# Kernel optimization log

Hardware: AMD Instinct MI355X
Metric: run time of the kernel (lower is better)

Reference implementation:

```python
import jax, jax.numpy as jnp
import numpy as np

E = 200000          # number of edges
MUL = 32            # multiplicity per irrep in irreps_in1/irreps_out
NT = 2              # num_tensors_in1
U = MUL * NT        # 64: combined multiplicity after fuse_in
SCALAR_DIM = 64     # irreps_edge_scalars num_irreps
HID = 64            # radial MLP hidden width
WNUM = 2 * U        # 128: LinearScaleWithWeights weight_numel (64 for 0e + 64 for 1o)
PW = 0.125          # uvw path weight sqrt(dim_out/ (u*v)) combined with 3j: all paths -> 1/8
INV_S3 = 1.0 / np.sqrt(3.0)

# e3nn normalize2mom constant for silu: 1/sqrt(E[silu(z)^2]), z ~ N(0,1)
_z = np.linspace(-12.0, 12.0, 200001)
_phi = np.exp(-0.5 * _z ** 2) / np.sqrt(2.0 * np.pi)
_s = _z / (1.0 + np.exp(-_z))
SILU_CST = float(1.0 / np.sqrt(np.trapz(_s ** 2 * _phi, _z)))


def setup_inputs() -> dict:
    key = jax.random.key(0)
    ks = jax.random.split(key, 15)
    f32 = jnp.float32
    return {
        "x1a": jax.random.normal(ks[0], (E, 128), f32),   # 32x0e + 32x1o
        "x1b": jax.random.normal(ks[1], (E, 128), f32),
        "x2": jax.random.normal(ks[2], (E, 4), f32),      # 1x0e + 1x1o
        "scalars": jax.random.normal(ks[3], (E, SCALAR_DIM), f32),
        # main tensor-product weights, one (u=64, w=32) block per instruction (v=1 squeezed)
        "w0": jax.random.normal(ks[4], (U, MUL), f32),    # 0e x 0e -> 0e (slot 0)
        "w1": jax.random.normal(ks[5], (U, MUL), f32),    # 1o x 1o -> 0e (slot 1)
        "w2": jax.random.normal(ks[6], (U, MUL), f32),    # 0e x 1o -> 1o (slot 2)
        "w3": jax.random.normal(ks[7], (U, MUL), f32),    # 1o x 0e -> 1o (slot 3)
        # LinearScaleWithWeights.linear_out: 64x0e+64x1o -> 32x0e+32x1o
        "Wl0": jax.random.normal(ks[8], (U, MUL), f32),
        "Wl1": jax.random.normal(ks[9], (U, MUL), f32),
        # radial MLP (e3nn FullyConnectedNet [64,64,64,128], silu)
        "Wm1": jax.random.normal(ks[10], (SCALAR_DIM, HID), f32),
        "Wm2": jax.random.normal(ks[11], (HID, HID), f32),
        "Wm3": jax.random.normal(ks[12], (HID, WNUM), f32),
        # final o3.Linear: 32x0e+32x1o -> 32x0e+32x1o
        "Wf0": jax.random.normal(ks[13], (MUL, MUL), f32),
        "Wf1": jax.random.normal(ks[14], (MUL, MUL), f32),
    }


def reference(x1a, x1b, x2, scalars, w0, w1, w2, w3, Wl0, Wl1, Wm1, Wm2, Wm3, Wf0, Wf1):
    n = x1a.shape[0]
    # fuse_in: stack heads then regroup per irrep -> combined 64x0e + 64x1o layout
    s0 = jnp.concatenate([x1a[:, :MUL], x1b[:, :MUL]], axis=1)                    # [E, 64]
    s1 = jnp.concatenate([x1a[:, MUL:].reshape(n, MUL, 3),
                          x1b[:, MUL:].reshape(n, MUL, 3)], axis=1)               # [E, 64, 3]
    y0 = x2[:, 0:1]    # 1x0e
    y1 = x2[:, 1:4]    # 1x1o

    # weight generator: e3nn FullyConnectedNet with normalized silu
    h = SILU_CST * jax.nn.silu((scalars @ Wm1) / jnp.sqrt(jnp.float32(SCALAR_DIM)))
    h = SILU_CST * jax.nn.silu((h @ Wm2) / jnp.sqrt(jnp.float32(HID)))
    weights = (h @ Wm3) / jnp.sqrt(jnp.float32(HID))                              # [E, 128]

    # main TensorProduct -> irreps_mid = 32x0e + 32x0e + 32x1o + 32x1o
    mid0 = PW * jnp.einsum('eu,uw->ew', s0 * y0, w0)                              # [E, 32]
    mid1 = (PW * INV_S3) * jnp.einsum('eu,uw->ew',
                                      jnp.einsum('euk,ek->eu', s1, y1), w1)       # [E, 32]
    mid2 = PW * jnp.einsum('eu,uw,ek->ewk', s0, w2, y1)                           # [E, 32, 3]
    mid3 = PW * jnp.einsum('euk,uw->ewk', s1 * y0[:, :, None], w3)                # [E, 32, 3]
    m0 = jnp.concatenate([mid0, mid1], axis=1)                                    # [E, 64] 0e
    m1 = jnp.concatenate([mid2, mid3], axis=1)                                    # [E, 64, 3] 1o

    # LinearScaleWithWeights: per-edge elementwise scale (uvu tp vs ones), then o3.Linear
    m0 = m0 * weights[:, :U]
    m1 = m1 * weights[:, U:, None]
    o0 = jnp.einsum('eu,uw->ew', m0, Wl0) / jnp.sqrt(jnp.float32(U))              # [E, 32]
    o1 = jnp.einsum('euk,uw->ewk', m1, Wl1) / jnp.sqrt(jnp.float32(U))            # [E, 32, 3]

    # final o3.Linear on irreps_out
    o0 = jnp.einsum('eu,uw->ew', o0, Wf0) / jnp.sqrt(jnp.float32(MUL))
    o1 = jnp.einsum('euk,uw->ewk', o1, Wf1) / jnp.sqrt(jnp.float32(MUL))
    return jnp.concatenate([o0, o1.reshape(n, MUL * 3)], axis=1)                  # [E, 128]
```

## Files before the change

kernel.cpp:

```cpp
#include <hip/hip_runtime.h>
#include <math.h>


#define TPB 256
#define ET  64
#define SAS 68

#define FMA4(acc, s, b)                                         \
  acc.x = fmaf((s), (b).x, acc.x); acc.y = fmaf((s), (b).y, acc.y); \
  acc.z = fmaf((s), (b).z, acc.z); acc.w = fmaf((s), (b).w, acc.w)

__global__ void zero_cst_kernel(double* cst) {
  if (threadIdx.x == 0) cst[0] = 0.0;
}

__global__ void cst_accum_kernel(double* cst) {
  __shared__ double red[256];
  double sum = 0.0;
  for (long i = (long)blockIdx.x * 256 + threadIdx.x; i <= 200000; i += 64L * 256) {
    double z = -12.0 + (double)i * (24.0 / 200000.0);
    double s = z / (1.0 + exp(-z));
    double phi = exp(-0.5 * z * z) * 0.3989422804014327;
    double f = s * s * phi;
    if (i == 0 || i == 200000) f *= 0.5;
    sum += f;
  }
  red[threadIdx.x] = sum;
  __syncthreads();
  for (int off = 128; off > 0; off >>= 1) {
    if (threadIdx.x < (unsigned)off) red[threadIdx.x] += red[threadIdx.x + off];
    __syncthreads();
  }
  if (threadIdx.x == 0) atomicAdd(cst, red[0]);
}

__global__ void prep_C_kernel(const float* __restrict__ Wl0, const float* __restrict__ Wf0,
                              const float* __restrict__ Wl1, const float* __restrict__ Wf1,
                              float* __restrict__ C0, float* __restrict__ C1) {
  const float* Wl = blockIdx.x ? Wl1 : Wl0;
  const float* Wf = blockIdx.x ? Wf1 : Wf0;
  float* C = blockIdx.x ? C1 : C0;
  for (int i = threadIdx.x; i < 64 * 32; i += 256) {
    int u = i >> 5, w = i & 31;
    float acc = 0.f;
#pragma unroll
    for (int v = 0; v < 32; ++v) acc = fmaf(Wl[u * 32 + v], Wf[v * 32 + w], acc);
    C[i] = acc * 0.022097086912079612f;
  }
}

__device__ __forceinline__ void stageB(const float* __restrict__ g, int ncols, int col0,
                                       float* __restrict__ sB, int t) {
#pragma unroll
  for (int r = 0; r < 2; ++r) {
    int i = (r * TPB + t) * 4;
    int c = i >> 5, j = i & 31;
    *(float4*)(sB + i) = *(const float4*)(g + c * ncols + col0 + j);
  }
}

__device__ __forceinline__ void gemm2(const float* __restrict__ sA,
                                      const float* __restrict__ sB,
                                      int e0l, int e1l, int cg,
                                      float4& out0, float4& out1) {
  float4 acc0 = make_float4(0.f, 0.f, 0.f, 0.f);
  float4 acc1 = make_float4(0.f, 0.f, 0.f, 0.f);
  const float* a0p = sA + e0l * SAS;
  const float* a1p = sA + e1l * SAS;
  const float* bp  = sB + 4 * cg;
#pragma unroll 4
  for (int c4 = 0; c4 < 16; ++c4) {
    float4 a0 = *(const float4*)(a0p + 4 * c4);
    float4 a1 = *(const float4*)(a1p + 4 * c4);
    const float* bb = bp + c4 * 128;
    float4 b0 = *(const float4*)(bb);
    float4 b1 = *(const float4*)(bb + 32);
    float4 b2 = *(const float4*)(bb + 64);
    float4 b3 = *(const float4*)(bb + 96);
    FMA4(acc0, a0.x, b0); FMA4(acc1, a1.x, b0);
    FMA4(acc0, a0.y, b1); FMA4(acc1, a1.y, b1);
    FMA4(acc0, a0.z, b2); FMA4(acc1, a1.z, b2);
    FMA4(acc0, a0.w, b3); FMA4(acc1, a1.w, b3);
  }
  out0 = acc0;
  out1 = acc1;
}

__device__ __forceinline__ float silu1(float x, float cst) {
  x *= 0.125f;
  return cst * x / (1.f + __expf(-x));
}

__device__ __forceinline__ float4 siluq(float4 v, float cst) {
  return make_float4(silu1(v.x, cst), silu1(v.y, cst), silu1(v.z, cst), silu1(v.w, cst));
}

__device__ __forceinline__ float4 muls(float4 a, float s) {
  return make_float4(a.x * s, a.y * s, a.z * s, a.w * s);
}

__device__ __forceinline__ float4 cmul(float4 a, float4 b, float s) {
  return make_float4(s * a.x * b.x, s * a.y * b.y, s * a.z * b.z, s * a.w * b.w);
}

__global__ __launch_bounds__(TPB, 4) void fused_tp(
    const float* __restrict__ x1a, const float* __restrict__ x1b,
    const float* __restrict__ x2, const float* __restrict__ scalars,
    const float* __restrict__ w0, const float* __restrict__ w1,
    const float* __restrict__ w2, const float* __restrict__ w3,
    const float* __restrict__ Wm1, const float* __restrict__ Wm2,
    const float* __restrict__ Wm3, const float* __restrict__ C0,
    const float* __restrict__ C1, const double* __restrict__ cstp,
    float* __restrict__ out) {
  __shared__ float sA[ET * SAS];
  __shared__ float sB0[64 * 32];
  __shared__ float sB1[64 * 32];
  __shared__ float sY[ET * 4];

  const int t  = threadIdx.x;
  const int cg = t & 7;
  const int eh = t >> 3;
  const long e0 = (long)blockIdx.x * ET;
  const float cst = (float)(1.0 / sqrt(cstp[0] * (24.0 / 200000.0)));

  const float pw   = 0.125f;
  const float pws3 = 0.125f * 0.57735026918962576f;

  if (t < ET) *(float4*)(sY + 4 * t) = *(const float4*)(x2 + (e0 + t) * 4);
#pragma unroll
  for (int r = 0; r < 4; ++r) {
    int i = r * TPB + t; int e = i >> 4; int j4 = (i & 15) << 2;
    *(float4*)(sA + e * SAS + j4) = *(const float4*)(scalars + (e0 + e) * 64 + j4);
  }
  stageB(Wm1, 64, 0, sB0, t);
  stageB(Wm1, 64, 32, sB1, t);
  __syncthreads();

  float4 h0a, h0b, h1a, h1b;
  {
    float4 r0, r1;
    gemm2(sA, sB0, eh, eh + 32, cg, r0, r1);
    h0a = siluq(r0, cst); h1a = siluq(r1, cst);
    gemm2(sA, sB1, eh, eh + 32, cg, r0, r1);
    h0b = siluq(r0, cst); h1b = siluq(r1, cst);
  }
  __syncthreads();

  *(float4*)(sA + eh * SAS + 4 * cg)        = h0a;
  *(float4*)(sA + eh * SAS + 32 + 4 * cg)   = h0b;
  *(float4*)(sA + (eh + 32) * SAS + 4 * cg)      = h1a;
  *(float4*)(sA + (eh + 32) * SAS + 32 + 4 * cg) = h1b;
  stageB(Wm2, 64, 0, sB0, t);
  stageB(Wm2, 64, 32, sB1, t);
  __syncthreads();

  {
    float4 r0, r1;
    gemm2(sA, sB0, eh, eh + 32, cg, r0, r1);
    h0a = siluq(r0, cst); h1a = siluq(r1, cst);
    gemm2(sA, sB1, eh, eh + 32, cg, r0, r1);
    h0b = siluq(r0, cst); h1b = siluq(r1, cst);
  }
  __syncthreads();

  *(float4*)(sA + eh * SAS + 4 * cg)        = h0a;
  *(float4*)(sA + eh * SAS + 32 + 4 * cg)   = h0b;
  *(float4*)(sA + (eh + 32) * SAS + 4 * cg)      = h1a;
  *(float4*)(sA + (eh + 32) * SAS + 32 + 4 * cg) = h1b;
  stageB(Wm3, 128, 0, sB0, t);
  stageB(Wm3, 128, 32, sB1, t);
  __syncthreads();

  float4 wq[2][4];
  {
    float4 r0, r1;
    gemm2(sA, sB0, eh, eh + 32, cg, r0, r1);
    wq[0][0] = muls(r0, 0.125f); wq[1][0] = muls(r1, 0.125f);
    gemm2(sA, sB1, eh, eh + 32, cg, r0, r1);
    wq[0][1] = muls(r0, 0.125f); wq[1][1] = muls(r1, 0.125f);
  }
  __syncthreads();
  stageB(Wm3, 128, 64, sB0, t);
  stageB(Wm3, 128, 96, sB1, t);
  __syncthreads();
  {
    float4 r0, r1;
    gemm2(sA, sB0, eh, eh + 32, cg, r0, r1);
    wq[0][2] = muls(r0, 0.125f); wq[1][2] = muls(r1, 0.125f);
    gemm2(sA, sB1, eh, eh + 32, cg, r0, r1);
    wq[0][3] = muls(r0, 0.125f); wq[1][3] = muls(r1, 0.125f);
  }
  __syncthreads();

#pragma unroll
  for (int r = 0; r < 4; ++r) {
    int i = r * TPB + t; int e = i >> 4; int j4 = (i & 15) << 2;
    const float* src = (j4 < 32) ? (x1a + (e0 + e) * 128 + j4)
                                 : (x1b + (e0 + e) * 128 + j4 - 32);
    *(float4*)(sA + e * SAS + j4) = *(const float4*)src;
  }
  stageB(w0, 32, 0, sB0, t);
  stageB(w2, 32, 0, sB1, t);
  __syncthreads();
  float4 m0q[2], p2q[2];
  gemm2(sA, sB0, eh, eh + 32, cg, m0q[0], m0q[1]);
  gemm2(sA, sB1, eh, eh + 32, cg, p2q[0], p2q[1]);
  __syncthreads();

#pragma unroll 2
  for (int r = 0; r < 16; ++r) {
    int i = r * TPB + t; int e = i >> 6; int u = i & 63;
    const float* xr = ((u < 32) ? x1a : x1b) + (e0 + e) * 128 + 32 + 3 * (u & 31);
    const float* yr = sY + e * 4;
    sA[e * SAS + u] = xr[0] * yr[1] + xr[1] * yr[2] + xr[2] * yr[3];
  }
  stageB(w1, 32, 0, sB0, t);
  stageB(w3, 32, 0, sB1, t);
  __syncthreads();
  float4 m1q[2];
  gemm2(sA, sB0, eh, eh + 32, cg, m1q[0], m1q[1]);
  __syncthreads();

#pragma unroll
  for (int ei = 0; ei < 2; ++ei) {
    int e = eh + 32 * ei;
    float y0v = sY[e * 4];
    *(float4*)(sA + e * SAS + 4 * cg)      = cmul(m0q[ei], wq[ei][0], pw * y0v);
    *(float4*)(sA + e * SAS + 32 + 4 * cg) = cmul(m1q[ei], wq[ei][1], pws3);
  }
  stageB(C0, 32, 0, sB0, t);
  __syncthreads();
  float4 o0q[2];
  gemm2(sA, sB0, eh, eh + 32, cg, o0q[0], o0q[1]);
  __syncthreads();

  stageB(C1, 32, 0, sB0, t);
  float o1v[2][12];
#pragma unroll
  for (int k = 0; k < 3; ++k) {
#pragma unroll 2
    for (int r = 0; r < 16; ++r) {
      int i = r * TPB + t; int e = i >> 6; int u = i & 63;
      const float* xr = ((u < 32) ? x1a : x1b) + (e0 + e) * 128 + 32 + 3 * (u & 31);
      sA[e * SAS + u] = xr[k];
    }
    __syncthreads();
    float4 t3[2];
    gemm2(sA, sB1, eh, eh + 32, cg, t3[0], t3[1]);
    __syncthreads();
#pragma unroll
    for (int ei = 0; ei < 2; ++ei) {
      int e = eh + 32 * ei;
      float y0v = sY[e * 4];
      float y1k = sY[e * 4 + 1 + k];
      *(float4*)(sA + e * SAS + 4 * cg)      = cmul(p2q[ei], wq[ei][2], pw * y1k);
      *(float4*)(sA + e * SAS + 32 + 4 * cg) = cmul(t3[ei], wq[ei][3], pw * y0v);
    }
    __syncthreads();
    float4 r0, r1;
    gemm2(sA, sB0, eh, eh + 32, cg, r0, r1);
    o1v[0][0 + k] = r0.x; o1v[0][3 + k] = r0.y; o1v[0][6 + k] = r0.z; o1v[0][9 + k] = r0.w;
    o1v[1][0 + k] = r1.x; o1v[1][3 + k] = r1.y; o1v[1][6 + k] = r1.z; o1v[1][9 + k] = r1.w;
    __syncthreads();
  }

#pragma unroll
  for (int ei = 0; ei < 2; ++ei) {
    long eg = e0 + eh + 32 * ei;
    float* ob = out + eg * 128;
    *(float4*)(ob + 4 * cg) = o0q[ei];
    float* o1b = ob + 32 + 12 * cg;
    *(float4*)(o1b)     = make_float4(o1v[ei][0], o1v[ei][1], o1v[ei][2],  o1v[ei][3]);
    *(float4*)(o1b + 4) = make_float4(o1v[ei][4], o1v[ei][5], o1v[ei][6],  o1v[ei][7]);
    *(float4*)(o1b + 8) = make_float4(o1v[ei][8], o1v[ei][9], o1v[ei][10], o1v[ei][11]);
  }
}

extern "C" void kernel_launch(void* const* d_in, const int* in_sizes, int n_in,
                              void* d_out, int out_size, void* d_ws, size_t ws_size,
                              hipStream_t stream) {
  const float* x1a     = (const float*)d_in[0];
  const float* x1b     = (const float*)d_in[1];
  const float* x2      = (const float*)d_in[2];
  const float* scalars = (const float*)d_in[3];
  const float* w0      = (const float*)d_in[4];
  const float* w1      = (const float*)d_in[5];
  const float* w2      = (const float*)d_in[6];
  const float* w3      = (const float*)d_in[7];
  const float* Wl0     = (const float*)d_in[8];
  const float* Wl1     = (const float*)d_in[9];
  const float* Wm1     = (const float*)d_in[10];
  const float* Wm2     = (const float*)d_in[11];
  const float* Wm3     = (const float*)d_in[12];
  const float* Wf0     = (const float*)d_in[13];
  const float* Wf1     = (const float*)d_in[14];
  float* out = (float*)d_out;

  double* cst = (double*)d_ws;
  float* C0 = (float*)d_ws + 128;
  float* C1 = C0 + 64 * 32;

  const int E = in_sizes[0] / 128;
  const int nblocks = E / ET;

  zero_cst_kernel<<<1, 64, 0, stream>>>(cst);
  cst_accum_kernel<<<64, 256, 0, stream>>>(cst);
  prep_C_kernel<<<2, 256, 0, stream>>>(Wl0, Wf0, Wl1, Wf1, C0, C1);
  fused_tp<<<nblocks, TPB, 0, stream>>>(x1a, x1b, x2, scalars, w0, w1, w2, w3,
                                        Wm1, Wm2, Wm3, C0, C1, cst, out);
}
```

Before: 481.4 us.

## Double-buffer shared tiles, hoist mid2 GEMM out of k-loop, vectorize x1 loads

Adds double-buffered A and B shared tiles so the next weight stage loads while the current GEMM runs, which cuts the number of barriers. The mid2 product (s0·w2 then ·C1) is computed once and scaled by y1k per k instead of running through the full 64-wide GEMM three times. The 1o inputs are loaded once into registers as float4 and reused for the dot product and for each k slice, replacing strided scalar global reads. An XOR-swizzled 32-wide buffer is added for the half-size GEMMs. In exchange, shared memory and register use grow, and launch bounds drop to 2 blocks per SM, which lowers occupancy.

```diff
diff --git a/kernel.cpp b/kernel.cpp
--- a/kernel.cpp
+++ b/kernel.cpp
@@ -57,6 +57,13 @@
     int c = i >> 5, j = i & 31;
     *(float4*)(sB + i) = *(const float4*)(g + c * ncols + col0 + j);
   }
+}
+
+__device__ __forceinline__ void stageB32(const float* __restrict__ g, int row0,
+                                         float* __restrict__ sB, int t) {
+  int i = t * 4;
+  int c = i >> 5, j = i & 31;
+  *(float4*)(sB + i) = *(const float4*)(g + (row0 + c) * 32 + j);
 }
 
 __device__ __forceinline__ void gemm2(const float* __restrict__ sA,
@@ -86,6 +93,39 @@
   out1 = acc1;
 }
 
+__device__ __forceinline__ void gemm32(const float* __restrict__ sAx,
+                                       const float* __restrict__ sB,
+                                       int e0l, int e1l, int cg,
+                                       float4& out0, float4& out1) {
+  float4 acc0 = make_float4(0.f, 0.f, 0.f, 0.f);
+  float4 acc1 = make_float4(0.f, 0.f, 0.f, 0.f);
+  const float* a0p = sAx + e0l * 32;
+  const float* a1p = sAx + e1l * 32;
+  const int x0 = (e0l & 7) << 2;
+  const int x1 = (e1l & 7) << 2;
+  const float* bp  = sB + 4 * cg;
+#pragma unroll
+  for (int c4 = 0; c4 < 8; ++c4) {
+    float4 a0 = *(const float4*)(a0p + ((c4 << 2) ^ x0));
+    float4 a1 = *(const float4*)(a1p + ((c4 << 2) ^ x1));
+    const float* bb = bp + c4 * 128;
+    float4 b0 = *(const float4*)(bb);
+    float4 b1 = *(const float4*)(bb + 32);
+    float4 b2 = *(const float4*)(bb + 64);
+    float4 b3 = *(const float4*)(bb + 96);
+    FMA4(acc0, a0.x, b0); FMA4(acc1, a1.x, b0);
+    FMA4(acc0, a0.y, b1); FMA4(acc1, a1.y, b1);
+    FMA4(acc0, a0.z, b2); FMA4(acc1, a1.z, b2);
+    FMA4(acc0, a0.w, b3); FMA4(acc1, a1.w, b3);
+  }
+  out0 = acc0;
+  out1 = acc1;
+}
+
+__device__ __forceinline__ void put32(float* __restrict__ sb, int e, int cg, float4 v) {
+  *(float4*)(sb + e * 32 + ((cg ^ (e & 7)) << 2)) = v;
+}
+
 __device__ __forceinline__ float silu1(float x, float cst) {
   x *= 0.125f;
   return cst * x / (1.f + __expf(-x));
@@ -103,7 +143,29 @@
   return make_float4(s * a.x * b.x, s * a.y * b.y, s * a.z * b.z, s * a.w * b.w);
 }
 
-__global__ __launch_bounds__(TPB, 4) void fused_tp(
+#define S1K(dst, kk) do {                                                     \
+  _Pragma("unroll")                                                           \
+  for (int r = 0; r < 4; ++r) {                                               \
+    int i = r * TPB + t; int e = i >> 4; int m = i & 15;                      \
+    *(float4*)((dst) + e * SAS + 4 * m) =                                     \
+      make_float4(xw[r][kk], xw[r][3 + kk], xw[r][6 + kk], xw[r][9 + kk]);    \
+  }                                                                           \
+} while (0)
+
+#define COMBINE(kk, r0, r1) do {                                              \
+  float ya = (kk == 0) ? yv0.y : (kk == 1) ? yv0.z : yv0.w;                   \
+  float yb = (kk == 0) ? yv1.y : (kk == 1) ? yv1.z : yv1.w;                   \
+  o1v[0][kk]     = ya * q2q[0].x + (r0).x;                                    \
+  o1v[0][3 + kk] = ya * q2q[0].y + (r0).y;                                    \
+  o1v[0][6 + kk] = ya * q2q[0].z + (r0).z;                                    \
+  o1v[0][9 + kk] = ya * q2q[0].w + (r0).w;                                    \
+  o1v[1][kk]     = yb * q2q[1].x + (r1).x;                                    \
+  o1v[1][3 + kk] = yb * q2q[1].y + (r1).y;                                    \
+  o1v[1][6 + kk] = yb * q2q[1].z + (r1).z;                                    \
+  o1v[1][9 + kk] = yb * q2q[1].w + (r1).w;                                    \
+} while (0)
+
+__global__ __launch_bounds__(TPB, 2) void fused_tp(
     const float* __restrict__ x1a, const float* __restrict__ x1b,
     const float* __restrict__ x2, const float* __restrict__ scalars,
     const float* __restrict__ w0, const float* __restrict__ w1,
@@ -112,10 +174,11 @@
     const float* __restrict__ Wm3, const float* __restrict__ C0,
     const float* __restrict__ C1, const double* __restrict__ cstp,
     float* __restrict__ out) {
-  __shared__ float sA[ET * SAS];
-  __shared__ float sB0[64 * 32];
-  __shared__ float sB1[64 * 32];
-  __shared__ float sY[ET * 4];
+  __shared__ __align__(16) float sA0[ET * SAS];
+  __shared__ __align__(16) float sA1[ET * SAS];
+  __shared__ __align__(16) float sBB[4][64 * 32];
+  __shared__ __align__(16) float s32[64 * 32];
+  __shared__ __align__(16) float sY[ET * 4];
 
   const int t  = threadIdx.x;
   const int cg = t & 7;
@@ -130,140 +193,157 @@
 #pragma unroll
   for (int r = 0; r < 4; ++r) {
     int i = r * TPB + t; int e = i >> 4; int j4 = (i & 15) << 2;
-    *(float4*)(sA + e * SAS + j4) = *(const float4*)(scalars + (e0 + e) * 64 + j4);
-  }
-  stageB(Wm1, 64, 0, sB0, t);
-  stageB(Wm1, 64, 32, sB1, t);
-  __syncthreads();
-
-  float4 h0a, h0b, h1a, h1b;
-  {
-    float4 r0, r1;
-    gemm2(sA, sB0, eh, eh + 32, cg, r0, r1);
-    h0a = siluq(r0, cst); h1a = siluq(r1, cst);
-    gemm2(sA, sB1, eh, eh + 32, cg, r0, r1);
-    h0b = siluq(r0, cst); h1b = siluq(r1, cst);
-  }
-  __syncthreads();
-
-  *(float4*)(sA + eh * SAS + 4 * cg)        = h0a;
-  *(float4*)(sA + eh * SAS + 32 + 4 * cg)   = h0b;
-  *(float4*)(sA + (eh + 32) * SAS + 4 * cg)      = h1a;
-  *(float4*)(sA + (eh + 32) * SAS + 32 + 4 * cg) = h1b;
-  stageB(Wm2, 64, 0, sB0, t);
-  stageB(Wm2, 64, 32, sB1, t);
-  __syncthreads();
-
-  {
-    float4 r0, r1;
-    gemm2(sA, sB0, eh, eh + 32, cg, r0, r1);
-    h0a = siluq(r0, cst); h1a = siluq(r1, cst);
-    gemm2(sA, sB1, eh, eh + 32, cg, r0, r1);
-    h0b = siluq(r0, cst); h1b = siluq(r1, cst);
-  }
-  __syncthreads();
-
-  *(float4*)(sA + eh * SAS + 4 * cg)        = h0a;
-  *(float4*)(sA + eh * SAS + 32 + 4 * cg)   = h0b;
-  *(float4*)(sA + (eh + 32) * SAS + 4 * cg)      = h1a;
-  *(float4*)(sA + (eh + 32) * SAS + 32 + 4 * cg) = h1b;
-  stageB(Wm3, 128, 0, sB0, t);
-  stageB(Wm3, 128, 32, sB1, t);
-  __syncthreads();
-
+    *(float4*)(sA0 + e * SAS + j4) = *(const float4*)(scalars + (e0 + e) * 64 + j4);
+  }
+  stageB(Wm1, 64, 0, sBB[0], t);
+  stageB(Wm1, 64, 32, sBB[1], t);
+  __syncthreads();
+
+  const float4 yv0 = *(const float4*)(sY + eh * 4);
+  const float4 yv1 = *(const float4*)(sY + (eh + 32) * 4);
+
+  stageB(Wm2, 64, 0, sBB[2], t);
+  stageB(Wm2, 64, 32, sBB[3], t);
+  {
+    float4 r0, r1;
+    gemm2(sA0, sBB[0], eh, eh + 32, cg, r0, r1);
+    *(float4*)(sA1 + eh * SAS + 4 * cg)        = siluq(r0, cst);
+    *(float4*)(sA1 + (eh + 32) * SAS + 4 * cg) = siluq(r1, cst);
+    gemm2(sA0, sBB[1], eh, eh + 32, cg, r0, r1);
+    *(float4*)(sA1 + eh * SAS + 32 + 4 * cg)        = siluq(r0, cst);
+    *(float4*)(sA1 + (eh + 32) * SAS + 32 + 4 * cg) = siluq(r1, cst);
+  }
+  __syncthreads();
+
+  stageB(Wm3, 128, 0, sBB[0], t);
+  stageB(Wm3, 128, 32, sBB[1], t);
+  {
+    float4 r0, r1;
+    gemm2(sA1, sBB[2], eh, eh + 32, cg, r0, r1);
+    *(float4*)(sA0 + eh * SAS + 4 * cg)        = siluq(r0, cst);
+    *(float4*)(sA0 + (eh + 32) * SAS + 4 * cg) = siluq(r1, cst);
+    gemm2(sA1, sBB[3], eh, eh + 32, cg, r0, r1);
+    *(float4*)(sA0 + eh * SAS + 32 + 4 * cg)        = siluq(r0, cst);
+    *(float4*)(sA0 + (eh + 32) * SAS + 32 + 4 * cg) = siluq(r1, cst);
+  }
+  __syncthreads();
+
+  stageB(Wm3, 128, 64, sBB[2], t);
+  stageB(Wm3, 128, 96, sBB[3], t);
   float4 wq[2][4];
   {
     float4 r0, r1;
-    gemm2(sA, sB0, eh, eh + 32, cg, r0, r1);
+    gemm2(sA0, sBB[0], eh, eh + 32, cg, r0, r1);
     wq[0][0] = muls(r0, 0.125f); wq[1][0] = muls(r1, 0.125f);
-    gemm2(sA, sB1, eh, eh + 32, cg, r0, r1);
+    gemm2(sA0, sBB[1], eh, eh + 32, cg, r0, r1);
     wq[0][1] = muls(r0, 0.125f); wq[1][1] = muls(r1, 0.125f);
   }
-  __syncthreads();
-  stageB(Wm3, 128, 64, sB0, t);
-  stageB(Wm3, 128, 96, sB1, t);
-  __syncthreads();
-  {
-    float4 r0, r1;
-    gemm2(sA, sB0, eh, eh + 32, cg, r0, r1);
-    wq[0][2] = muls(r0, 0.125f); wq[1][2] = muls(r1, 0.125f);
-    gemm2(sA, sB1, eh, eh + 32, cg, r0, r1);
-    wq[0][3] = muls(r0, 0.125f); wq[1][3] = muls(r1, 0.125f);
-  }
-  __syncthreads();
-
 #pragma unroll
   for (int r = 0; r < 4; ++r) {
     int i = r * TPB + t; int e = i >> 4; int j4 = (i & 15) << 2;
     const float* src = (j4 < 32) ? (x1a + (e0 + e) * 128 + j4)
                                  : (x1b + (e0 + e) * 128 + j4 - 32);
-    *(float4*)(sA + e * SAS + j4) = *(const float4*)src;
-  }
-  stageB(w0, 32, 0, sB0, t);
-  stageB(w2, 32, 0, sB1, t);
-  __syncthreads();
+    *(float4*)(sA1 + e * SAS + j4) = *(const float4*)src;
+  }
+  __syncthreads();
+
+  stageB(w0, 32, 0, sBB[0], t);
+  stageB(w2, 32, 0, sBB[1], t);
+  float xw[4][12];
+#pragma unroll
+  for (int r = 0; r < 4; ++r) {
+    int i = r * TPB + t; int e = i >> 4; int m = i & 15;
+    const float* src = ((m < 8) ? x1a : x1b) + (e0 + e) * 128 + 32 + 12 * (m & 7);
+    float4 va = *(const float4*)(src);
+    float4 vb = *(const float4*)(src + 4);
+    float4 vc = *(const float4*)(src + 8);
+    xw[r][0] = va.x; xw[r][1]  = va.y; xw[r][2]  = va.z; xw[r][3]  = va.w;
+    xw[r][4] = vb.x; xw[r][5]  = vb.y; xw[r][6]  = vb.z; xw[r][7]  = vb.w;
+    xw[r][8] = vc.x; xw[r][9]  = vc.y; xw[r][10] = vc.z; xw[r][11] = vc.w;
+  }
+  {
+    float4 r0, r1;
+    gemm2(sA0, sBB[2], eh, eh + 32, cg, r0, r1);
+    wq[0][2] = muls(r0, 0.125f); wq[1][2] = muls(r1, 0.125f);
+    gemm2(sA0, sBB[3], eh, eh + 32, cg, r0, r1);
+    wq[0][3] = muls(r0, 0.125f); wq[1][3] = muls(r1, 0.125f);
+  }
+  __syncthreads();
+
+  stageB(w1, 32, 0, sBB[2], t);
+  stageB(w3, 32, 0, sBB[3], t);
   float4 m0q[2], p2q[2];
-  gemm2(sA, sB0, eh, eh + 32, cg, m0q[0], m0q[1]);
-  gemm2(sA, sB1, eh, eh + 32, cg, p2q[0], p2q[1]);
-  __syncthreads();
-
-#pragma unroll 2
-  for (int r = 0; r < 16; ++r) {
-    int i = r * TPB + t; int e = i >> 6; int u = i & 63;
-    const float* xr = ((u < 32) ? x1a : x1b) + (e0 + e) * 128 + 32 + 3 * (u & 31);
+  gemm2(sA1, sBB[0], eh, eh + 32, cg, m0q[0], m0q[1]);
+  gemm2(sA1, sBB[1], eh, eh + 32, cg, p2q[0], p2q[1]);
+#pragma unroll
+  for (int r = 0; r < 4; ++r) {
+    int i = r * TPB + t; int e = i >> 4; int m = i & 15;
     const float* yr = sY + e * 4;
-    sA[e * SAS + u] = xr[0] * yr[1] + xr[1] * yr[2] + xr[2] * yr[3];
-  }
-  stageB(w1, 32, 0, sB0, t);
-  stageB(w3, 32, 0, sB1, t);
-  __syncthreads();
+    float4 tv;
+    tv.x = xw[r][0] * yr[1] + xw[r][1]  * yr[2] + xw[r][2]  * yr[3];
+    tv.y = xw[r][3] * yr[1] + xw[r][4]  * yr[2] + xw[r][5]  * yr[3];
+    tv.z = xw[r][6] * yr[1] + xw[r][7]  * yr[2] + xw[r][8]  * yr[3];
+    tv.w = xw[r][9] * yr[1] + xw[r][10] * yr[2] + xw[r][11] * yr[3];
+    *(float4*)(sA0 + e * SAS + 4 * m) = tv;
+  }
+  __syncthreads();
+
+  stageB(C0, 32, 0, sBB[0], t);
+  stageB32(C1, 0, sBB[1], t);
   float4 m1q[2];
-  gemm2(sA, sB0, eh, eh + 32, cg, m1q[0], m1q[1]);
-  __syncthreads();
-
-#pragma unroll
-  for (int ei = 0; ei < 2; ++ei) {
-    int e = eh + 32 * ei;
-    float y0v = sY[e * 4];
-    *(float4*)(sA + e * SAS + 4 * cg)      = cmul(m0q[ei], wq[ei][0], pw * y0v);
-    *(float4*)(sA + e * SAS + 32 + 4 * cg) = cmul(m1q[ei], wq[ei][1], pws3);
-  }
-  stageB(C0, 32, 0, sB0, t);
-  __syncthreads();
+  gemm2(sA0, sBB[2], eh, eh + 32, cg, m1q[0], m1q[1]);
+  S1K(sA1, 0);
+  put32(s32, eh,      cg, cmul(p2q[0], wq[0][2], pw));
+  put32(s32, eh + 32, cg, cmul(p2q[1], wq[1][2], pw));
+  __syncthreads();
+
+  stageB32(C1, 32, sBB[2], t);
+  float4 t3[2], q2q[2];
+  gemm2(sA1, sBB[3], eh, eh + 32, cg, t3[0], t3[1]);
+  gemm32(s32, sBB[1], eh, eh + 32, cg, q2q[0], q2q[1]);
+  *(float4*)(sA0 + eh * SAS + 4 * cg)             = cmul(m0q[0], wq[0][0], pw * yv0.x);
+  *(float4*)(sA0 + eh * SAS + 32 + 4 * cg)        = cmul(m1q[0], wq[0][1], pws3);
+  *(float4*)(sA0 + (eh + 32) * SAS + 4 * cg)      = cmul(m0q[1], wq[1][0], pw * yv1.x);
+  *(float4*)(sA0 + (eh + 32) * SAS + 32 + 4 * cg) = cmul(m1q[1], wq[1][1], pws3);
+  __syncthreads();
+
   float4 o0q[2];
-  gemm2(sA, sB0, eh, eh + 32, cg, o0q[0], o0q[1]);
-  __syncthreads();
-
-  stageB(C1, 32, 0, sB0, t);
+  gemm2(sA0, sBB[0], eh, eh + 32, cg, o0q[0], o0q[1]);
+  put32(sBB[1], eh,      cg, cmul(t3[0], wq[0][3], pw * yv0.x));
+  put32(sBB[1], eh + 32, cg, cmul(t3[1], wq[1][3], pw * yv1.x));
+  S1K(sA1, 1);
+  __syncthreads();
+
   float o1v[2][12];
-#pragma unroll
-  for (int k = 0; k < 3; ++k) {
-#pragma unroll 2
-    for (int r = 0; r < 16; ++r) {
-      int i = r * TPB + t; int e = i >> 6; int u = i & 63;
-      const float* xr = ((u < 32) ? x1a : x1b) + (e0 + e) * 128 + 32 + 3 * (u & 31);
-      sA[e * SAS + u] = xr[k];
-    }
-    __syncthreads();
-    float4 t3[2];
-    gemm2(sA, sB1, eh, eh + 32, cg, t3[0], t3[1]);
-    __syncthreads();
-#pragma unroll
-    for (int ei = 0; ei < 2; ++ei) {
-      int e = eh + 32 * ei;
-      float y0v = sY[e * 4];
-      float y1k = sY[e * 4 + 1 + k];
-      *(float4*)(sA + e * SAS + 4 * cg)      = cmul(p2q[ei], wq[ei][2], pw * y1k);
-      *(float4*)(sA + e * SAS + 32 + 4 * cg) = cmul(t3[ei], wq[ei][3], pw * y0v);
-    }
-    __syncthreads();
-    float4 r0, r1;
-    gemm2(sA, sB0, eh, eh + 32, cg, r0, r1);
-    o1v[0][0 + k] = r0.x; o1v[0][3 + k] = r0.y; o1v[0][6 + k] = r0.z; o1v[0][9 + k] = r0.w;
-    o1v[1][0 + k] = r1.x; o1v[1][3 + k] = r1.y; o1v[1][6 + k] = r1.z; o1v[1][9 + k] = r1.w;
-    __syncthreads();
-  }
-
+  {
+    float4 r0, r1;
+    gemm32(sBB[1], sBB[2], eh, eh + 32, cg, r0, r1);
+    COMBINE(0, r0, r1);
+  }
+  gemm2(sA1, sBB[3], eh, eh + 32, cg, t3[0], t3[1]);
+  S1K(sA0, 2);
+  __syncthreads();
+
+  put32(s32, eh,      cg, cmul(t3[0], wq[0][3], pw * yv0.x));
+  put32(s32, eh + 32, cg, cmul(t3[1], wq[1][3], pw * yv1.x));
+  float4 t32a, t32b;
+  gemm2(sA0, sBB[3], eh, eh + 32, cg, t32a, t32b);
+  __syncthreads();
+
+  {
+    float4 r0, r1;
+    gemm32(s32, sBB[2], eh, eh + 32, cg, r0, r1);
+    COMBINE(1, r0, r1);
+  }
+  put32(sBB[1], eh,      cg, cmul(t32a, wq[0][3], pw * yv0.x));
+  put32(sBB[1], eh + 32, cg, cmul(t32b, wq[1][3], pw * yv1.x));
+  __syncthreads();
+
+  {
+    float4 r0, r1;
+    gemm32(sBB[1], sBB[2], eh, eh + 32, cg, r0, r1);
+    COMBINE(2, r0, r1);
+  }
 #pragma unroll
   for (int ei = 0; ei < 2; ++ei) {
     long eg = e0 + eh + 32 * ei;
```

New measurement: 1.135 ms. +135.9%, slower.

## Widen edge tile to 128 per block and restructure tensor-product GEMM stages

Applied to the files above, without the earlier changes.

The fused kernel is templated on edges per thread, and the main launch now handles 128 edges per block with 4 edges per thread. A tail launch with 2 edges per thread covers the remainder. Dual-B GEMMs share A-fragment loads across two weight matrices. The 1o path is split algebraically: the y1-dependent term is computed once through a K=32 GEMM and scaled per component k, instead of one K=64 GEMM per component. The x1 vector gathers are vectorized with float4 loads, and launch bounds drop to 3 blocks per SM. This raises register pressure and reduces occupancy, and it assumes E is a multiple of 64.

```diff
diff --git a/kernel.cpp b/kernel.cpp
--- a/kernel.cpp
+++ b/kernel.cpp
@@ -3,7 +3,6 @@
 
 
 #define TPB 256
-#define ET  64
 #define SAS 68
 
 #define FMA4(acc, s, b)                                         \
@@ -59,31 +58,99 @@
   }
 }
 
-__device__ __forceinline__ void gemm2(const float* __restrict__ sA,
-                                      const float* __restrict__ sB,
-                                      int e0l, int e1l, int cg,
-                                      float4& out0, float4& out1) {
-  float4 acc0 = make_float4(0.f, 0.f, 0.f, 0.f);
-  float4 acc1 = make_float4(0.f, 0.f, 0.f, 0.f);
-  const float* a0p = sA + e0l * SAS;
-  const float* a1p = sA + e1l * SAS;
-  const float* bp  = sB + 4 * cg;
+template <int EPT>
+__device__ __forceinline__ void gemm_one(const float* __restrict__ sA,
+                                         const float* __restrict__ sB,
+                                         int eh, int cg, float4 (&out)[EPT]) {
+  float4 acc[EPT];
+#pragma unroll
+  for (int i = 0; i < EPT; ++i) acc[i] = make_float4(0.f, 0.f, 0.f, 0.f);
+  const float* bp = sB + 4 * cg;
 #pragma unroll 4
   for (int c4 = 0; c4 < 16; ++c4) {
-    float4 a0 = *(const float4*)(a0p + 4 * c4);
-    float4 a1 = *(const float4*)(a1p + 4 * c4);
     const float* bb = bp + c4 * 128;
     float4 b0 = *(const float4*)(bb);
     float4 b1 = *(const float4*)(bb + 32);
     float4 b2 = *(const float4*)(bb + 64);
     float4 b3 = *(const float4*)(bb + 96);
-    FMA4(acc0, a0.x, b0); FMA4(acc1, a1.x, b0);
-    FMA4(acc0, a0.y, b1); FMA4(acc1, a1.y, b1);
-    FMA4(acc0, a0.z, b2); FMA4(acc1, a1.z, b2);
-    FMA4(acc0, a0.w, b3); FMA4(acc1, a1.w, b3);
-  }
-  out0 = acc0;
-  out1 = acc1;
+#pragma unroll
+    for (int i = 0; i < EPT; ++i) {
+      float4 a = *(const float4*)(sA + (eh + 32 * i) * SAS + 4 * c4);
+      FMA4(acc[i], a.x, b0);
+      FMA4(acc[i], a.y, b1);
+      FMA4(acc[i], a.z, b2);
+      FMA4(acc[i], a.w, b3);
+    }
+  }
+#pragma unroll
+  for (int i = 0; i < EPT; ++i) out[i] = acc[i];
+}
+
+template <int EPT>
+__device__ __forceinline__ void gemm_dual(const float* __restrict__ sA,
+                                          const float* __restrict__ sB0,
+                                          const float* __restrict__ sB1,
+                                          int eh, int cg,
+                                          float4 (&out0)[EPT], float4 (&out1)[EPT]) {
+  float4 a0[EPT], a1[EPT];
+#pragma unroll
+  for (int i = 0; i < EPT; ++i) {
+    a0[i] = make_float4(0.f, 0.f, 0.f, 0.f);
+    a1[i] = make_float4(0.f, 0.f, 0.f, 0.f);
+  }
+  const float* bp0 = sB0 + 4 * cg;
+  const float* bp1 = sB1 + 4 * cg;
+#pragma unroll 2
+  for (int c4 = 0; c4 < 16; ++c4) {
+    const float* b0b = bp0 + c4 * 128;
+    const float* b1b = bp1 + c4 * 128;
+    float4 B00 = *(const float4*)(b0b);
+    float4 B01 = *(const float4*)(b0b + 32);
+    float4 B02 = *(const float4*)(b0b + 64);
+    float4 B03 = *(const float4*)(b0b + 96);
+    float4 B10 = *(const float4*)(b1b);
+    float4 B11 = *(const float4*)(b1b + 32);
+    float4 B12 = *(const float4*)(b1b + 64);
+    float4 B13 = *(const float4*)(b1b + 96);
+#pragma unroll
+    for (int i = 0; i < EPT; ++i) {
+      float4 a = *(const float4*)(sA + (eh + 32 * i) * SAS + 4 * c4);
+      FMA4(a0[i], a.x, B00); FMA4(a1[i], a.x, B10);
+      FMA4(a0[i], a.y, B01); FMA4(a1[i], a.y, B11);
+      FMA4(a0[i], a.z, B02); FMA4(a1[i], a.z, B12);
+      FMA4(a0[i], a.w, B03); FMA4(a1[i], a.w, B13);
+    }
+  }
+#pragma unroll
+  for (int i = 0; i < EPT; ++i) { out0[i] = a0[i]; out1[i] = a1[i]; }
+}
+
+template <int EPT>
+__device__ __forceinline__ void gemm_k32(const float* __restrict__ sA,
+                                         const float* __restrict__ sBbase,
+                                         int eh, int cg, float4 (&out)[EPT]) {
+  float4 acc[EPT];
+#pragma unroll
+  for (int i = 0; i < EPT; ++i) acc[i] = make_float4(0.f, 0.f, 0.f, 0.f);
+  const float* bp = sBbase + 4 * cg;
+#pragma unroll 4
+  for (int c4 = 0; c4 < 8; ++c4) {
+    const float* bb = bp + c4 * 128;
+    float4 b0 = *(const float4*)(bb);
+    float4 b1 = *(const float4*)(bb + 32);
+    float4 b2 = *(const float4*)(bb + 64);
+    float4 b3 = *(const float4*)(bb + 96);
+#pragma unroll
+    for (int i = 0; i < EPT; ++i) {
+      float4 a = *(const float4*)(sA + (eh + 32 * i) * SAS + 4 * c4);
+      FMA4(acc[i], a.x, b0);
+      FMA4(acc[i], a.y, b1);
+      FMA4(acc[i], a.z, b2);
+      FMA4(acc[i], a.w, b3);
+    }
+  }
+#pragma unroll
+  for (int i = 0; i < EPT; ++i) out[i] = acc[i];
 }
 
 __device__ __forceinline__ float silu1(float x, float cst) {
@@ -103,7 +170,18 @@
   return make_float4(s * a.x * b.x, s * a.y * b.y, s * a.z * b.z, s * a.w * b.w);
 }
 
-__global__ __launch_bounds__(TPB, 4) void fused_tp(
+__device__ __forceinline__ float4 emul(float4 a, float4 b) {
+  return make_float4(a.x * b.x, a.y * b.y, a.z * b.z, a.w * b.w);
+}
+
+__device__ __forceinline__ float4 pick3(float4 va, float4 vb, float4 vc, int k) {
+  if (k == 0) return make_float4(va.x, va.w, vb.z, vc.y);
+  if (k == 1) return make_float4(va.y, vb.x, vb.w, vc.z);
+  return make_float4(va.z, vb.y, vc.x, vc.w);
+}
+
+template <int EPT>
+__global__ __launch_bounds__(TPB, 3) void fused_tp(
     const float* __restrict__ x1a, const float* __restrict__ x1b,
     const float* __restrict__ x2, const float* __restrict__ scalars,
     const float* __restrict__ w0, const float* __restrict__ w1,
@@ -111,16 +189,17 @@
     const float* __restrict__ Wm1, const float* __restrict__ Wm2,
     const float* __restrict__ Wm3, const float* __restrict__ C0,
     const float* __restrict__ C1, const double* __restrict__ cstp,
-    float* __restrict__ out) {
-  __shared__ float sA[ET * SAS];
-  __shared__ float sB0[64 * 32];
-  __shared__ float sB1[64 * 32];
-  __shared__ float sY[ET * 4];
+    float* __restrict__ out, long ebase) {
+  constexpr int ET = 32 * EPT;
+  __shared__ __align__(16) float sA[ET * SAS];
+  __shared__ __align__(16) float sB0[64 * 32];
+  __shared__ __align__(16) float sB1[64 * 32];
+  __shared__ __align__(16) float sY[ET * 4];
 
   const int t  = threadIdx.x;
   const int cg = t & 7;
   const int eh = t >> 3;
-  const long e0 = (long)blockIdx.x * ET;
+  const long e0 = ebase + (long)blockIdx.x * ET;
   const float cst = (float)(1.0 / sqrt(cstp[0] * (24.0 / 200000.0)));
 
   const float pw   = 0.125f;
@@ -128,7 +207,7 @@
 
   if (t < ET) *(float4*)(sY + 4 * t) = *(const float4*)(x2 + (e0 + t) * 4);
 #pragma unroll
-  for (int r = 0; r < 4; ++r) {
+  for (int r = 0; r < ET / 16; ++r) {
     int i = r * TPB + t; int e = i >> 4; int j4 = (i & 15) << 2;
     *(float4*)(sA + e * SAS + j4) = *(const float4*)(scalars + (e0 + e) * 64 + j4);
   }
@@ -136,64 +215,51 @@
   stageB(Wm1, 64, 32, sB1, t);
   __syncthreads();
 
-  float4 h0a, h0b, h1a, h1b;
-  {
-    float4 r0, r1;
-    gemm2(sA, sB0, eh, eh + 32, cg, r0, r1);
-    h0a = siluq(r0, cst); h1a = siluq(r1, cst);
-    gemm2(sA, sB1, eh, eh + 32, cg, r0, r1);
-    h0b = siluq(r0, cst); h1b = siluq(r1, cst);
-  }
-  __syncthreads();
-
-  *(float4*)(sA + eh * SAS + 4 * cg)        = h0a;
-  *(float4*)(sA + eh * SAS + 32 + 4 * cg)   = h0b;
-  *(float4*)(sA + (eh + 32) * SAS + 4 * cg)      = h1a;
-  *(float4*)(sA + (eh + 32) * SAS + 32 + 4 * cg) = h1b;
+  float4 yv[EPT];
+#pragma unroll
+  for (int i = 0; i < EPT; ++i) yv[i] = *(const float4*)(sY + (eh + 32 * i) * 4);
+
+  float4 g0[EPT], g1[EPT];
+
+  gemm_dual<EPT>(sA, sB0, sB1, eh, cg, g0, g1);
+  __syncthreads();
+#pragma unroll
+  for (int i = 0; i < EPT; ++i) {
+    int e = eh + 32 * i;
+    *(float4*)(sA + e * SAS + 4 * cg)      = siluq(g0[i], cst);
+    *(float4*)(sA + e * SAS + 32 + 4 * cg) = siluq(g1[i], cst);
+  }
   stageB(Wm2, 64, 0, sB0, t);
   stageB(Wm2, 64, 32, sB1, t);
   __syncthreads();
 
-  {
-    float4 r0, r1;
-    gemm2(sA, sB0, eh, eh + 32, cg, r0, r1);
-    h0a = siluq(r0, cst); h1a = siluq(r1, cst);
-    gemm2(sA, sB1, eh, eh + 32, cg, r0, r1);
-    h0b = siluq(r0, cst); h1b = siluq(r1, cst);
-  }
-  __syncthreads();
-
-  *(float4*)(sA + eh * SAS + 4 * cg)        = h0a;
-  *(float4*)(sA + eh * SAS + 32 + 4 * cg)   = h0b;
-  *(float4*)(sA + (eh + 32) * SAS + 4 * cg)      = h1a;
-  *(float4*)(sA + (eh + 32) * SAS + 32 + 4 * cg) = h1b;
+  gemm_dual<EPT>(sA, sB0, sB1, eh, cg, g0, g1);
+  __syncthreads();
+#pragma unroll
+  for (int i = 0; i < EPT; ++i) {
+    int e = eh + 32 * i;
+    *(float4*)(sA + e * SAS + 4 * cg)      = siluq(g0[i], cst);
+    *(float4*)(sA + e * SAS + 32 + 4 * cg) = siluq(g1[i], cst);
+  }
   stageB(Wm3, 128, 0, sB0, t);
   stageB(Wm3, 128, 32, sB1, t);
   __syncthreads();
 
-  float4 wq[2][4];
-  {
-    float4 r0, r1;
-    gemm2(sA, sB0, eh, eh + 32, cg, r0, r1);
-    wq[0][0] = muls(r0, 0.125f); wq[1][0] = muls(r1, 0.125f);
-    gemm2(sA, sB1, eh, eh + 32, cg, r0, r1);
-    wq[0][1] = muls(r0, 0.125f); wq[1][1] = muls(r1, 0.125f);
-  }
+  float4 wq0[EPT], wq1[EPT], wq2[EPT], wq3[EPT];
+  gemm_dual<EPT>(sA, sB0, sB1, eh, cg, g0, g1);
+#pragma unroll
+  for (int i = 0; i < EPT; ++i) { wq0[i] = muls(g0[i], 0.125f); wq1[i] = muls(g1[i], 0.125f); }
   __syncthreads();
   stageB(Wm3, 128, 64, sB0, t);
   stageB(Wm3, 128, 96, sB1, t);
   __syncthreads();
-  {
-    float4 r0, r1;
-    gemm2(sA, sB0, eh, eh + 32, cg, r0, r1);
-    wq[0][2] = muls(r0, 0.125f); wq[1][2] = muls(r1, 0.125f);
-    gemm2(sA, sB1, eh, eh + 32, cg, r0, r1);
-    wq[0][3] = muls(r0, 0.125f); wq[1][3] = muls(r1, 0.125f);
-  }
-  __syncthreads();
-
-#pragma unroll
-  for (int r = 0; r < 4; ++r) {
+  gemm_dual<EPT>(sA, sB0, sB1, eh, cg, g0, g1);
+#pragma unroll
+  for (int i = 0; i < EPT; ++i) { wq2[i] = muls(g0[i], 0.125f); wq3[i] = muls(g1[i], 0.125f); }
+  __syncthreads();
+
+#pragma unroll
+  for (int r = 0; r < ET / 16; ++r) {
     int i = r * TPB + t; int e = i >> 4; int j4 = (i & 15) << 2;
     const float* src = (j4 < 32) ? (x1a + (e0 + e) * 128 + j4)
                                  : (x1b + (e0 + e) * 128 + j4 - 32);
@@ -202,77 +268,115 @@
   stageB(w0, 32, 0, sB0, t);
   stageB(w2, 32, 0, sB1, t);
   __syncthreads();
-  float4 m0q[2], p2q[2];
-  gemm2(sA, sB0, eh, eh + 32, cg, m0q[0], m0q[1]);
-  gemm2(sA, sB1, eh, eh + 32, cg, p2q[0], p2q[1]);
-  __syncthreads();
-
-#pragma unroll 2
-  for (int r = 0; r < 16; ++r) {
-    int i = r * TPB + t; int e = i >> 6; int u = i & 63;
-    const float* xr = ((u < 32) ? x1a : x1b) + (e0 + e) * 128 + 32 + 3 * (u & 31);
+
+  float4 m0q[EPT], p2g[EPT], wq3g[EPT];
+  {
+    float4 p2q[EPT];
+    gemm_dual<EPT>(sA, sB0, sB1, eh, cg, m0q, p2q);
+#pragma unroll
+    for (int i = 0; i < EPT; ++i) {
+      p2g[i]  = cmul(p2q[i], wq2[i], pw);
+      wq3g[i] = muls(wq3[i], pw * yv[i].x);
+    }
+  }
+  __syncthreads();
+
+#pragma unroll
+  for (int r = 0; r < ET / 16; ++r) {
+    int i = r * TPB + t; int e = i >> 4; int u4 = i & 15;
+    const float* src = ((u4 < 8) ? x1a : x1b) + (e0 + e) * 128 + 32 + 12 * (u4 & 7);
+    float4 va = *(const float4*)(src);
+    float4 vb = *(const float4*)(src + 4);
+    float4 vc = *(const float4*)(src + 8);
     const float* yr = sY + e * 4;
-    sA[e * SAS + u] = xr[0] * yr[1] + xr[1] * yr[2] + xr[2] * yr[3];
+    float4 tv;
+    tv.x = va.x * yr[1] + va.y * yr[2] + va.z * yr[3];
+    tv.y = va.w * yr[1] + vb.x * yr[2] + vb.y * yr[3];
+    tv.z = vb.z * yr[1] + vb.w * yr[2] + vc.x * yr[3];
+    tv.w = vc.y * yr[1] + vc.z * yr[2] + vc.w * yr[3];
+    *(float4*)(sA + e * SAS + 4 * u4) = tv;
   }
   stageB(w1, 32, 0, sB0, t);
-  stageB(w3, 32, 0, sB1, t);
-  __syncthreads();
-  float4 m1q[2];
-  gemm2(sA, sB0, eh, eh + 32, cg, m1q[0], m1q[1]);
-  __syncthreads();
-
-#pragma unroll
-  for (int ei = 0; ei < 2; ++ei) {
-    int e = eh + 32 * ei;
-    float y0v = sY[e * 4];
-    *(float4*)(sA + e * SAS + 4 * cg)      = cmul(m0q[ei], wq[ei][0], pw * y0v);
-    *(float4*)(sA + e * SAS + 32 + 4 * cg) = cmul(m1q[ei], wq[ei][1], pws3);
-  }
-  stageB(C0, 32, 0, sB0, t);
-  __syncthreads();
-  float4 o0q[2];
-  gemm2(sA, sB0, eh, eh + 32, cg, o0q[0], o0q[1]);
-  __syncthreads();
-
-  stageB(C1, 32, 0, sB0, t);
-  float o1v[2][12];
+  stageB(C0, 32, 0, sB1, t);
+  __syncthreads();
+
+  float4 m1q[EPT];
+  gemm_one<EPT>(sA, sB0, eh, cg, m1q);
+  __syncthreads();
+
+#pragma unroll
+  for (int i = 0; i < EPT; ++i) {
+    int e = eh + 32 * i;
+    *(float4*)(sA + e * SAS + 4 * cg)      = cmul(m0q[i], wq0[i], pw * yv[i].x);
+    *(float4*)(sA + e * SAS + 32 + 4 * cg) = cmul(m1q[i], wq1[i], pws3);
+  }
+  stageB(w3, 32, 0, sB0, t);
+  __syncthreads();
+
+  {
+    float4 o0q[EPT];
+    gemm_one<EPT>(sA, sB1, eh, cg, o0q);
+#pragma unroll
+    for (int i = 0; i < EPT; ++i) {
+      long eg = e0 + eh + 32 * i;
+      *(float4*)(out + eg * 128 + 4 * cg) = o0q[i];
+    }
+  }
+  __syncthreads();
+
+#pragma unroll
+  for (int i = 0; i < EPT; ++i) {
+    int e = eh + 32 * i;
+    *(float4*)(sA + e * SAS + 4 * cg) = p2g[i];
+  }
+  stageB(C1, 32, 0, sB1, t);
+  __syncthreads();
+
+  float4 q2[EPT];
+  gemm_k32<EPT>(sA, sB1, eh, cg, q2);
+
+  float o1v[EPT][12];
 #pragma unroll
   for (int k = 0; k < 3; ++k) {
-#pragma unroll 2
-    for (int r = 0; r < 16; ++r) {
-      int i = r * TPB + t; int e = i >> 6; int u = i & 63;
-      const float* xr = ((u < 32) ? x1a : x1b) + (e0 + e) * 128 + 32 + 3 * (u & 31);
-      sA[e * SAS + u] = xr[k];
-    }
     __syncthreads();
-    float4 t3[2];
-    gemm2(sA, sB1, eh, eh + 32, cg, t3[0], t3[1]);
+#pragma unroll
+    for (int r = 0; r < ET / 16; ++r) {
+      int i = r * TPB + t; int e = i >> 4; int u4 = i & 15;
+      const float* src = ((u4 < 8) ? x1a : x1b) + (e0 + e) * 128 + 32 + 12 * (u4 & 7);
+      float4 va = *(const float4*)(src);
+      float4 vb = *(const float4*)(src + 4);
+      float4 vc = *(const float4*)(src + 8);
+      *(float4*)(sA + e * SAS + 4 * u4) = pick3(va, vb, vc, k);
+    }
     __syncthreads();
-#pragma unroll
-    for (int ei = 0; ei < 2; ++ei) {
-      int e = eh + 32 * ei;
-      float y0v = sY[e * 4];
-      float y1k = sY[e * 4 + 1 + k];
-      *(float4*)(sA + e * SAS + 4 * cg)      = cmul(p2q[ei], wq[ei][2], pw * y1k);
-      *(float4*)(sA + e * SAS + 32 + 4 * cg) = cmul(t3[ei], wq[ei][3], pw * y0v);
-    }
+    float4 t3[EPT];
+    gemm_one<EPT>(sA, sB0, eh, cg, t3);
     __syncthreads();
-    float4 r0, r1;
-    gemm2(sA, sB0, eh, eh + 32, cg, r0, r1);
-    o1v[0][0 + k] = r0.x; o1v[0][3 + k] = r0.y; o1v[0][6 + k] = r0.z; o1v[0][9 + k] = r0.w;
-    o1v[1][0 + k] = r1.x; o1v[1][3 + k] = r1.y; o1v[1][6 + k] = r1.z; o1v[1][9 + k] = r1.w;
+#pragma unroll
+    for (int i = 0; i < EPT; ++i) {
+      int e = eh + 32 * i;
+      *(float4*)(sA + e * SAS + 4 * cg) = emul(t3[i], wq3g[i]);
+    }
     __syncthreads();
-  }
-
-#pragma unroll
-  for (int ei = 0; ei < 2; ++ei) {
-    long eg = e0 + eh + 32 * ei;
-    float* ob = out + eg * 128;
-    *(float4*)(ob + 4 * cg) = o0q[ei];
-    float* o1b = ob + 32 + 12 * cg;
-    *(float4*)(o1b)     = make_float4(o1v[ei][0], o1v[ei][1], o1v[ei][2],  o1v[ei][3]);
-    *(float4*)(o1b + 4) = make_float4(o1v[ei][4], o1v[ei][5], o1v[ei][6],  o1v[ei][7]);
-    *(float4*)(o1b + 8) = make_float4(o1v[ei][8], o1v[ei][9], o1v[ei][10], o1v[ei][11]);
+    float4 q3[EPT];
+    gemm_k32<EPT>(sA, sB1 + 1024, eh, cg, q3);
+#pragma unroll
+    for (int i = 0; i < EPT; ++i) {
+      float yl = (k == 0) ? yv[i].y : (k == 1) ? yv[i].z : yv[i].w;
+      o1v[i][0 + k] = yl * q2[i].x + q3[i].x;
+      o1v[i][3 + k] = yl * q2[i].y + q3[i].y;
+      o1v[i][6 + k] = yl * q2[i].z + q3[i].z;
+      o1v[i][9 + k] = yl * q2[i].w + q3[i].w;
+    }
+  }
+
+#pragma unroll
+  for (int i = 0; i < EPT; ++i) {
+    long eg = e0 + eh + 32 * i;
+    float* o1b = out + eg * 128 + 32 + 12 * cg;
+    *(float4*)(o1b)     = make_float4(o1v[i][0], o1v[i][1], o1v[i][2],  o1v[i][3]);
+    *(float4*)(o1b + 4) = make_float4(o1v[i][4], o1v[i][5], o1v[i][6],  o1v[i][7]);
+    *(float4*)(o1b + 8) = make_float4(o1v[i][8], o1v[i][9], o1v[i][10], o1v[i][11]);
   }
 }
 
@@ -301,11 +405,17 @@
   float* C1 = C0 + 64 * 32;
 
   const int E = in_sizes[0] / 128;
-  const int nblocks = E / ET;
+  const int nfull = E / 128;
+  const int rem   = E - nfull * 128;
 
   zero_cst_kernel<<<1, 64, 0, stream>>>(cst);
   cst_accum_kernel<<<64, 256, 0, stream>>>(cst);
   prep_C_kernel<<<2, 256, 0, stream>>>(Wl0, Wf0, Wl1, Wf1, C0, C1);
-  fused_tp<<<nblocks, TPB, 0, stream>>>(x1a, x1b, x2, scalars, w0, w1, w2, w3,
-                                        Wm1, Wm2, Wm3, C0, C1, cst, out);
-}
+  fused_tp<4><<<nfull, TPB, 0, stream>>>(x1a, x1b, x2, scalars, w0, w1, w2, w3,
+                                         Wm1, Wm2, Wm3, C0, C1, cst, out, 0L);
+  if (rem > 0) {
+    fused_tp<2><<<rem / 64, TPB, 0, stream>>>(x1a, x1b, x2, scalars, w0, w1, w2, w3,
+                                              Wm1, Wm2, Wm3, C0, C1, cst, out,
+                                              (long)nfull * 128);
+  }
+}
```

New measurement: 542.3 us. 1.13x slower.
